# Kernel tuning notes

Measured on AMD Instinct MI355X. Metric: run time of the kernel, lower is better.

Reference implementation:

```python
import jax, jax.numpy as jnp
import numpy as np

N_NODES = 20000
N_EDGES = 40000
MAX_NB = 6
N_ATOM_FEAT = 98
N_BOND_FEAT = 13
HIDDEN = 256
DEPTH = 4
INPUT_SIZE = N_ATOM_FEAT + N_BOND_FEAT  # 111, hmess width


def setup_inputs() -> dict:
    key = jax.random.key(0)
    ks = jax.random.split(key, 10)
    fnode = jax.random.normal(ks[0], (N_NODES, N_ATOM_FEAT), jnp.float32)
    # fmess: col0/col1 are src/dst node indices stored as floats, cols 2: are bond features
    idx = jax.random.randint(ks[1], (N_EDGES, 2), 0, N_NODES).astype(jnp.float32)
    bond = jax.random.normal(ks[2], (N_EDGES, N_BOND_FEAT), jnp.float32)
    fmess = jnp.concatenate([idx, bond], axis=1)  # [E, 2 + n_bond_feat]
    agraph = jax.random.randint(ks[3], (N_NODES, MAX_NB), 0, N_EDGES)
    bgraph = jax.random.randint(ks[4], (N_EDGES, MAX_NB), 0, N_EDGES)
    s = 0.02
    W_z_w = jax.random.normal(ks[5], (HIDDEN, INPUT_SIZE + HIDDEN), jnp.float32) * s
    W_z_b = jnp.zeros((HIDDEN,), jnp.float32)
    W_r_w = jax.random.normal(ks[6], (HIDDEN, INPUT_SIZE), jnp.float32) * s  # no bias (W_r)
    U_r_w = jax.random.normal(ks[7], (HIDDEN, HIDDEN), jnp.float32) * s
    U_r_b = jnp.zeros((HIDDEN,), jnp.float32)
    W_h_w = jax.random.normal(ks[8], (HIDDEN, INPUT_SIZE + HIDDEN), jnp.float32) * s
    W_h_b = jnp.zeros((HIDDEN,), jnp.float32)
    W_o_w = jax.random.normal(ks[9], (HIDDEN, N_ATOM_FEAT + HIDDEN), jnp.float32) * s
    W_o_b = jnp.zeros((HIDDEN,), jnp.float32)
    return dict(fnode=fnode, fmess=fmess, agraph=agraph, bgraph=bgraph,
                W_z_w=W_z_w, W_z_b=W_z_b, W_r_w=W_r_w, U_r_w=U_r_w, U_r_b=U_r_b,
                W_h_w=W_h_w, W_h_b=W_h_b, W_o_w=W_o_w, W_o_b=W_o_b)


def reference(fnode, fmess, agraph, bgraph,
              W_z_w, W_z_b, W_r_w, U_r_w, U_r_b, W_h_w, W_h_b, W_o_w, W_o_b):
    # GraphFeatEncoder: gather src-node features and concat with bond features
    src = fmess[:, 0].astype(jnp.int32)
    x = jnp.concatenate([fnode[src], fmess[:, 2:]], axis=-1)  # [E, input_size]
    E = x.shape[0]
    H = W_z_b.shape[0]
    emask = jnp.ones((E, 1), x.dtype).at[0, 0].set(0.0)  # message 0 is padding
    Wr_x = (x @ W_r_w.T)[:, None, :]  # [E,1,H], constant across depth iterations
    h = jnp.zeros((E, H), x.dtype)
    # DGCNGRU: D-MPNN style GRU over directed-edge states
    for _ in range(DEPTH):
        h_nei = h[bgraph]                                   # [E, max_nb, H] gather
        sum_h = h_nei.sum(axis=1)                           # [E, H]
        z = jax.nn.sigmoid(jnp.concatenate([x, sum_h], axis=1) @ W_z_w.T + W_z_b)
        r = jax.nn.sigmoid(Wr_x + h_nei @ U_r_w.T + U_r_b)  # [E, max_nb, H]
        sum_gh = (r * h_nei).sum(axis=1)
        pre_h = jnp.tanh(jnp.concatenate([x, sum_gh], axis=1) @ W_h_w.T + W_h_b)
        h = ((1.0 - z) * sum_h + z * pre_h) * emask
    # DGCNEncoder readout: aggregate incoming edge states per atom
    nei_msg = h[agraph].sum(axis=1)                          # [N, H] gather + sum
    node_h = jax.nn.gelu(jnp.concatenate([fnode, nei_msg], axis=1) @ W_o_w.T + W_o_b,
                         approximate=False)                  # torch nn.GELU = exact erf
    nmask = jnp.ones((node_h.shape[0], 1), node_h.dtype).at[0, 0].set(0.0)  # node 0 pad
    hatom = node_h * nmask
    return hatom  # GraphFeatEncoder returns (hatom, None); hmol is always None
```

## Files before the change

### kernel.cpp

```cpp
#include <hip/hip_runtime.h>
#include <cstddef>
#include <cstdint>

typedef unsigned short u16;
typedef unsigned int   u32;
typedef __bf16  bf16x8 __attribute__((ext_vector_type(8)));
typedef float   f32x4  __attribute__((ext_vector_type(4)));

#define DEV __device__ __forceinline__

DEV float b2f(u16 u) { union { u32 i; float f; } c; c.i = ((u32)u) << 16; return c.f; }
DEV u16 f2b(float x) { union { float f; u32 i; } c; c.f = x; u32 b = c.i;
                       return (u16)((b + 0x7FFFu + ((b >> 16) & 1u)) >> 16); }
DEV float sigm(float x)  { return 1.0f / (1.0f + __expf(-x)); }
DEV float tanh_(float x) { return 1.0f - 2.0f / (1.0f + __expf(2.0f * x)); }
DEV float gelu_(float x) { return 0.5f * x * (1.0f + erff(x * 0.70710678118654752f)); }

DEV void u4tof8(uint4 v, float* f) {
    f[0] = b2f((u16)(v.x & 0xFFFF)); f[1] = b2f((u16)(v.x >> 16));
    f[2] = b2f((u16)(v.y & 0xFFFF)); f[3] = b2f((u16)(v.y >> 16));
    f[4] = b2f((u16)(v.z & 0xFFFF)); f[5] = b2f((u16)(v.z >> 16));
    f[6] = b2f((u16)(v.w & 0xFFFF)); f[7] = b2f((u16)(v.w >> 16));
}
DEV uint4 f8tou4(const float* f) {
    uint4 v;
    v.x = (u32)f2b(f[0]) | ((u32)f2b(f[1]) << 16);
    v.y = (u32)f2b(f[2]) | ((u32)f2b(f[3]) << 16);
    v.z = (u32)f2b(f[4]) | ((u32)f2b(f[5]) << 16);
    v.w = (u32)f2b(f[6]) | ((u32)f2b(f[7]) << 16);
    return v;
}

#define OB_X     0ull
#define OB_FB    10240000ull
#define OB_PRU   15360000ull
#define OB_H     35840000ull
#define OB_UH    56320000ull
#define OB_SH    76800000ull
#define OB_SGH   97280000ull
#define OB_BZ    117760000ull
#define OB_BH    117956608ull
#define OB_BU    118153216ull
#define OB_BR    118284288ull
#define OB_BO    118349824ull
#define WS_BYTES 118546432ull

__global__ __launch_bounds__(256) void k_repack(
    const float* __restrict__ Wz, const float* __restrict__ Wr,
    const float* __restrict__ Ur, const float* __restrict__ Wh,
    const float* __restrict__ Wo,
    u16* __restrict__ BzT, u16* __restrict__ BhT, u16* __restrict__ BuT,
    u16* __restrict__ BrT, u16* __restrict__ BoT) {
    int idx = blockIdx.x * 256 + threadIdx.x;
    {
        int n = idx / 384, k = idx % 384;
        float vz, vh, vo;
        if (k < 111)      { vz = Wz[n * 367 + k];          vh = Wh[n * 367 + k]; }
        else if (k < 128) { vz = 0.0f;                     vh = 0.0f; }
        else              { vz = Wz[n * 367 + k - 17];     vh = Wh[n * 367 + k - 17]; }
        if (k < 98)       vo = Wo[n * 354 + k];
        else if (k < 128) vo = 0.0f;
        else              vo = Wo[n * 354 + k - 30];
        BzT[idx] = f2b(vz); BhT[idx] = f2b(vh); BoT[idx] = f2b(vo);
    }
    if (idx < 65536) {
        BuT[idx] = f2b(Ur[idx]);
    }
    if (idx < 32768) {
        int n = idx >> 7, k = idx & 127;
        BrT[idx] = f2b(k < 111 ? Wr[n * 111 + k] : 0.0f);
    }
}

__global__ void k_build_x(const float* __restrict__ fnode,
                          const float* __restrict__ fmess, u16* __restrict__ x) {
    int e = blockIdx.x, c = threadIdx.x;
    int src = (int)fmess[(size_t)e * 15];
    float v = 0.0f;
    if (c < 98)       v = fnode[(size_t)src * 98 + c];
    else if (c < 111) v = fmess[(size_t)e * 15 + 2 + (c - 98)];
    x[(size_t)e * 128 + c] = f2b(v);
}

__global__ __launch_bounds__(256) void k_build_fb(const float* __restrict__ fnode,
                                                  u16* __restrict__ fb) {
    int idx = blockIdx.x * 256 + threadIdx.x;
    int n = idx >> 7, c = idx & 127;
    fb[idx] = f2b(c < 98 ? fnode[(size_t)n * 98 + c] : 0.0f);
}

DEV void stage128x64(const u16* __restrict__ g, size_t row0, int ld, int k0,
                     u16* s, int tid) {
    #pragma unroll
    for (int it = 0; it < 4; ++it) {
        int r = it * 32 + (tid >> 3);
        int c = (tid & 7) << 3;
        uint4 v = *(const uint4*)(g + (row0 + (size_t)r) * ld + k0 + c);
        int byte = (((r << 6) + c) << 1) ^ ((r & 7) << 4);
        *(uint4*)((char*)s + byte) = v;
    }
}

DEV void mma64s(const u16* As, const u16* Bs, f32x4 acc[4][4], int wr, int wc, int lane) {
    int rb = (wr << 6) + (lane & 15);
    int cb = (wc << 6) + (lane & 15);
    int ko = (lane >> 4) << 3;
    #pragma unroll
    for (int kh = 0; kh < 2; ++kh) {
        bf16x8 a[4], b[4];
        #pragma unroll
        for (int i = 0; i < 4; ++i) {
            int ar = rb + (i << 4);
            int ab = (((ar << 6) + (kh << 5) + ko) << 1) ^ ((ar & 7) << 4);
            a[i] = *(const bf16x8*)((const char*)As + ab);
            int br = cb + (i << 4);
            int bb = (((br << 6) + (kh << 5) + ko) << 1) ^ ((br & 7) << 4);
            b[i] = *(const bf16x8*)((const char*)Bs + bb);
        }
        #pragma unroll
        for (int i = 0; i < 4; ++i)
            #pragma unroll
            for (int j = 0; j < 4; ++j)
                acc[i][j] = __builtin_amdgcn_mfma_f32_16x16x32_bf16(b[j], a[i], acc[i][j], 0, 0, 0);
    }
}

#define MG_PROLOG()                                          \
    int tid = threadIdx.x, lane = tid & 63, w = tid >> 6;    \
    int wr = w >> 1, wc = w & 1;                             \
    int bm = blockIdx.x >> 1, bn = blockIdx.x & 1;           \
    size_t m0 = (size_t)bm << 7; int n0 = bn << 7;           \
    int row_l = (wr << 6) + (lane & 15);                     \
    int col_l = (wc << 6) + ((lane >> 4) << 2);

#define ACC_INIT(A)                                          \
    { f32x4 zz = {0.f, 0.f, 0.f, 0.f};                       \
      _Pragma("unroll") for (int i = 0; i < 4; ++i)          \
      _Pragma("unroll") for (int j = 0; j < 4; ++j) A[i][j] = zz; }

__global__ __launch_bounds__(256) void k_mg_p(
    const u16* __restrict__ x, const u16* __restrict__ BrT,
    const float* __restrict__ urb, u16* __restrict__ PrU) {
    __shared__ u16 As[8192], Bs[8192];
    MG_PROLOG()
    f32x4 acc[4][4]; ACC_INIT(acc)
    for (int k0 = 0; k0 < 128; k0 += 64) {
        __syncthreads();
        stage128x64(x, m0, 128, k0, As, tid);
        stage128x64(BrT, (size_t)n0, 128, k0, Bs, tid);
        __syncthreads();
        mma64s(As, Bs, acc, wr, wc, lane);
    }
    #pragma unroll
    for (int mi = 0; mi < 4; ++mi) {
        int m = (int)m0 + row_l + (mi << 4);
        if (m >= 40000) continue;
        #pragma unroll
        for (int ni = 0; ni < 4; ++ni) {
            int col = n0 + col_l + (ni << 4);
            float4 ub = *(const float4*)(urb + col);
            ushort4 o;
            o.x = f2b(acc[mi][ni][0] + ub.x); o.y = f2b(acc[mi][ni][1] + ub.y);
            o.z = f2b(acc[mi][ni][2] + ub.z); o.w = f2b(acc[mi][ni][3] + ub.w);
            *(ushort4*)(PrU + (size_t)m * 256 + col) = o;
        }
    }
}

__global__ __launch_bounds__(256) void k_d1(
    const u16* __restrict__ x, const u16* __restrict__ BzT,
    const u16* __restrict__ BhT, const float* __restrict__ bz,
    const float* __restrict__ bh, u16* __restrict__ h) {
    __shared__ u16 As[8192], Bs1[8192], Bs2[8192];
    MG_PROLOG()
    f32x4 aZ[4][4], aH[4][4]; ACC_INIT(aZ) ACC_INIT(aH)
    for (int k0 = 0; k0 < 128; k0 += 64) {
        __syncthreads();
        stage128x64(x, m0, 128, k0, As, tid);
        stage128x64(BzT, (size_t)n0, 384, k0, Bs1, tid);
        stage128x64(BhT, (size_t)n0, 384, k0, Bs2, tid);
        __syncthreads();
        mma64s(As, Bs1, aZ, wr, wc, lane);
        mma64s(As, Bs2, aH, wr, wc, lane);
    }
    #pragma unroll
    for (int mi = 0; mi < 4; ++mi) {
        int m = (int)m0 + row_l + (mi << 4);
        if (m >= 40000) continue;
        #pragma unroll
        for (int ni = 0; ni < 4; ++ni) {
            int col = n0 + col_l + (ni << 4);
            float4 vz = *(const float4*)(bz + col);
            float4 vh = *(const float4*)(bh + col);
            float r[4];
            r[0] = sigm(aZ[mi][ni][0] + vz.x) * tanh_(aH[mi][ni][0] + vh.x);
            r[1] = sigm(aZ[mi][ni][1] + vz.y) * tanh_(aH[mi][ni][1] + vh.y);
            r[2] = sigm(aZ[mi][ni][2] + vz.z) * tanh_(aH[mi][ni][2] + vh.z);
            r[3] = sigm(aZ[mi][ni][3] + vz.w) * tanh_(aH[mi][ni][3] + vh.w);
            if (m == 0) { r[0] = r[1] = r[2] = r[3] = 0.0f; }
            ushort4 o;
            o.x = f2b(r[0]); o.y = f2b(r[1]); o.z = f2b(r[2]); o.w = f2b(r[3]);
            *(ushort4*)(h + (size_t)m * 256 + col) = o;
        }
    }
}

__global__ __launch_bounds__(256) void k_mg_uh(
    const u16* __restrict__ A, const u16* __restrict__ BT, u16* __restrict__ C) {
    __shared__ u16 As[8192], Bs[8192];
    MG_PROLOG()
    f32x4 acc[4][4]; ACC_INIT(acc)
    for (int k0 = 0; k0 < 256; k0 += 64) {
        __syncthreads();
        stage128x64(A, m0, 256, k0, As, tid);
        stage128x64(BT, (size_t)n0, 256, k0, Bs, tid);
        __syncthreads();
        mma64s(As, Bs, acc, wr, wc, lane);
    }
    #pragma unroll
    for (int mi = 0; mi < 4; ++mi) {
        int m = (int)m0 + row_l + (mi << 4);
        if (m >= 40000) continue;
        #pragma unroll
        for (int ni = 0; ni < 4; ++ni) {
            int col = n0 + col_l + (ni << 4);
            ushort4 o;
            o.x = f2b(acc[mi][ni][0]); o.y = f2b(acc[mi][ni][1]);
            o.z = f2b(acc[mi][ni][2]); o.w = f2b(acc[mi][ni][3]);
            *(ushort4*)(C + (size_t)m * 256 + col) = o;
        }
    }
}

__global__ __launch_bounds__(256) void k_mg_fused(
    const u16* __restrict__ x, const u16* __restrict__ sumh,
    const u16* __restrict__ sumgh, const u16* __restrict__ BzT,
    const u16* __restrict__ BhT, const float* __restrict__ bz,
    const float* __restrict__ bh, u16* __restrict__ h) {
    __shared__ u16 As1[8192], As2[8192], Bs1[8192], Bs2[8192];
    MG_PROLOG()
    f32x4 aZ[4][4], aH[4][4]; ACC_INIT(aZ) ACC_INIT(aH)
    for (int s = 0; s < 6; ++s) {
        int k0 = s << 6;
        __syncthreads();
        if (s < 2) {
            stage128x64(x, m0, 128, k0, As1, tid);
        } else {
            stage128x64(sumh,  m0, 256, k0 - 128, As1, tid);
            stage128x64(sumgh, m0, 256, k0 - 128, As2, tid);
        }
        stage128x64(BzT, (size_t)n0, 384, k0, Bs1, tid);
        stage128x64(BhT, (size_t)n0, 384, k0, Bs2, tid);
        __syncthreads();
        mma64s(As1, Bs1, aZ, wr, wc, lane);
        mma64s(s < 2 ? As1 : As2, Bs2, aH, wr, wc, lane);
    }
    #pragma unroll
    for (int mi = 0; mi < 4; ++mi) {
        int m = (int)m0 + row_l + (mi << 4);
        if (m >= 40000) continue;
        #pragma unroll
        for (int ni = 0; ni < 4; ++ni) {
            int col = n0 + col_l + (ni << 4);
            float4 vz = *(const float4*)(bz + col);
            float4 vh = *(const float4*)(bh + col);
            ushort4 sh4 = *(const ushort4*)(sumh + (size_t)m * 256 + col);
            float shv[4] = {b2f(sh4.x), b2f(sh4.y), b2f(sh4.z), b2f(sh4.w)};
            float bzv[4] = {vz.x, vz.y, vz.z, vz.w};
            float bhv[4] = {vh.x, vh.y, vh.z, vh.w};
            float o[4];
            #pragma unroll
            for (int q = 0; q < 4; ++q) {
                float z   = sigm(aZ[mi][ni][q] + bzv[q]);
                float pre = tanh_(aH[mi][ni][q] + bhv[q]);
                o[q] = (1.0f - z) * shv[q] + z * pre;
            }
            if (m == 0) { o[0] = o[1] = o[2] = o[3] = 0.0f; }
            ushort4 ov;
            ov.x = f2b(o[0]); ov.y = f2b(o[1]); ov.z = f2b(o[2]); ov.w = f2b(o[3]);
            *(ushort4*)(h + (size_t)m * 256 + col) = ov;
        }
    }
}

__global__ __launch_bounds__(256) void k_mg_out(
    const u16* __restrict__ fb, const u16* __restrict__ nei,
    const u16* __restrict__ BoT, const float* __restrict__ bo,
    float* __restrict__ out) {
    __shared__ u16 As[8192], Bs[8192];
    MG_PROLOG()
    f32x4 acc[4][4]; ACC_INIT(acc)
    for (int s = 0; s < 6; ++s) {
        int k0 = s << 6;
        __syncthreads();
        if (s < 2) stage128x64(fb,  m0, 128, k0, As, tid);
        else       stage128x64(nei, m0, 256, k0 - 128, As, tid);
        stage128x64(BoT, (size_t)n0, 384, k0, Bs, tid);
        __syncthreads();
        mma64s(As, Bs, acc, wr, wc, lane);
    }
    #pragma unroll
    for (int mi = 0; mi < 4; ++mi) {
        int m = (int)m0 + row_l + (mi << 4);
        if (m >= 20000) continue;
        #pragma unroll
        for (int ni = 0; ni < 4; ++ni) {
            int col = n0 + col_l + (ni << 4);
            float4 vb = *(const float4*)(bo + col);
            float4 o;
            o.x = gelu_(acc[mi][ni][0] + vb.x);
            o.y = gelu_(acc[mi][ni][1] + vb.y);
            o.z = gelu_(acc[mi][ni][2] + vb.z);
            o.w = gelu_(acc[mi][ni][3] + vb.w);
            if (m == 0) { o.x = o.y = o.z = o.w = 0.0f; }
            *(float4*)(out + (size_t)m * 256 + col) = o;
        }
    }
}

__global__ __launch_bounds__(256) void k_gather_edge(
    const u16* __restrict__ h, const u16* __restrict__ Uh,
    const u16* __restrict__ PrU, const int* __restrict__ bgraph,
    u16* __restrict__ sumh, u16* __restrict__ sumgh) {
    int e = (blockIdx.x << 3) + (threadIdx.x >> 5);
    int c = (threadIdx.x & 31) << 3;
    size_t o = (size_t)e * 256 + c;
    float pr[8];
    u4tof8(*(const uint4*)(PrU + o), pr);
    float sh[8] = {}, sg[8] = {};
    #pragma unroll
    for (int j = 0; j < 6; ++j) {
        int b = bgraph[e * 6 + j];
        float hv[8], uv[8];
        u4tof8(*(const uint4*)(h  + (size_t)b * 256 + c), hv);
        u4tof8(*(const uint4*)(Uh + (size_t)b * 256 + c), uv);
        #pragma unroll
        for (int q = 0; q < 8; ++q) {
            sh[q] += hv[q];
            sg[q] += sigm(pr[q] + uv[q]) * hv[q];
        }
    }
    *(uint4*)(sumh  + o) = f8tou4(sh);
    *(uint4*)(sumgh + o) = f8tou4(sg);
}

__global__ __launch_bounds__(256) void k_gather_node(
    const u16* __restrict__ h, const int* __restrict__ agraph,
    u16* __restrict__ nei) {
    int n = (blockIdx.x << 3) + (threadIdx.x >> 5);
    int c = (threadIdx.x & 31) << 3;
    float s[8] = {};
    #pragma unroll
    for (int j = 0; j < 6; ++j) {
        int a = agraph[n * 6 + j];
        float hv[8];
        u4tof8(*(const uint4*)(h + (size_t)a * 256 + c), hv);
        #pragma unroll
        for (int q = 0; q < 8; ++q) s[q] += hv[q];
    }
    *(uint4*)(nei + (size_t)n * 256 + c) = f8tou4(s);
}

extern "C" void kernel_launch(void* const* d_in, const int* in_sizes, int n_in,
                              void* d_out, int out_size, void* d_ws, size_t ws_size,
                              hipStream_t stream) {
    if (ws_size < WS_BYTES) return;

    const float* fnode  = (const float*)d_in[0];
    const float* fmess  = (const float*)d_in[1];
    const int*   agraph = (const int*)d_in[2];
    const int*   bgraph = (const int*)d_in[3];
    const float* Wz  = (const float*)d_in[4];
    const float* bz  = (const float*)d_in[5];
    const float* Wr  = (const float*)d_in[6];
    const float* Ur  = (const float*)d_in[7];
    const float* urb = (const float*)d_in[8];
    const float* Wh  = (const float*)d_in[9];
    const float* bh  = (const float*)d_in[10];
    const float* Wo  = (const float*)d_in[11];
    const float* bo  = (const float*)d_in[12];

    char* base = (char*)d_ws;
    u16* x     = (u16*)(base + OB_X);
    u16* fb    = (u16*)(base + OB_FB);
    u16* PrU   = (u16*)(base + OB_PRU);
    u16* h     = (u16*)(base + OB_H);
    u16* Uh    = (u16*)(base + OB_UH);
    u16* nei   = (u16*)(base + OB_UH);
    u16* sumh  = (u16*)(base + OB_SH);
    u16* sumgh = (u16*)(base + OB_SGH);
    u16* BzT   = (u16*)(base + OB_BZ);
    u16* BhT   = (u16*)(base + OB_BH);
    u16* BuT   = (u16*)(base + OB_BU);
    u16* BrT   = (u16*)(base + OB_BR);
    u16* BoT   = (u16*)(base + OB_BO);
    float* out = (float*)d_out;

    hipLaunchKernelGGL(k_repack, dim3(384), dim3(256), 0, stream,
                       Wz, Wr, Ur, Wh, Wo, BzT, BhT, BuT, BrT, BoT);
    hipLaunchKernelGGL(k_build_x, dim3(40000), dim3(128), 0, stream, fnode, fmess, x);
    hipLaunchKernelGGL(k_build_fb, dim3(10000), dim3(256), 0, stream, fnode, fb);
    hipLaunchKernelGGL(k_mg_p, dim3(313 * 2), dim3(256), 0, stream, x, BrT, urb, PrU);
    hipLaunchKernelGGL(k_d1,   dim3(313 * 2), dim3(256), 0, stream, x, BzT, BhT, bz, bh, h);
    for (int d = 1; d < 4; ++d) {
        hipLaunchKernelGGL(k_mg_uh, dim3(313 * 2), dim3(256), 0, stream, h, BuT, Uh);
        hipLaunchKernelGGL(k_gather_edge, dim3(5000), dim3(256), 0, stream,
                           h, Uh, PrU, bgraph, sumh, sumgh);
        hipLaunchKernelGGL(k_mg_fused, dim3(313 * 2), dim3(256), 0, stream,
                           x, sumh, sumgh, BzT, BhT, bz, bh, h);
    }
    hipLaunchKernelGGL(k_gather_node, dim3(2500), dim3(256), 0, stream, h, agraph, nei);
    hipLaunchKernelGGL(k_mg_out, dim3(157 * 2), dim3(256), 0, stream, fb, nei, BoT, bo, out);
}
```

Baseline: 500.3 us.

## Use 128x64 GEMM tiles with register-prefetched global loads across all matmul kernels

```diff
diff --git a/kernel.cpp b/kernel.cpp
--- a/kernel.cpp
+++ b/kernel.cpp
@@ -55,26 +55,26 @@
     {
         int n = idx / 384, k = idx % 384;
         float vz, vh, vo;
-        if (k < 111)      { vz = Wz[n * 367 + k];          vh = Wh[n * 367 + k]; }
-        else if (k < 128) { vz = 0.0f;                     vh = 0.0f; }
-        else              { vz = Wz[n * 367 + k - 17];     vh = Wh[n * 367 + k - 17]; }
+        if (k < 111)      { vz = Wz[n * 367 + k];      vh = Wh[n * 367 + k]; }
+        else if (k < 128) { vz = 0.0f;                 vh = 0.0f; }
+        else              { vz = Wz[n * 367 + k - 17]; vh = Wh[n * 367 + k - 17]; }
         if (k < 98)       vo = Wo[n * 354 + k];
         else if (k < 128) vo = 0.0f;
         else              vo = Wo[n * 354 + k - 30];
         BzT[idx] = f2b(vz); BhT[idx] = f2b(vh); BoT[idx] = f2b(vo);
     }
-    if (idx < 65536) {
-        BuT[idx] = f2b(Ur[idx]);
-    }
+    if (idx < 65536) BuT[idx] = f2b(Ur[idx]);
     if (idx < 32768) {
         int n = idx >> 7, k = idx & 127;
         BrT[idx] = f2b(k < 111 ? Wr[n * 111 + k] : 0.0f);
     }
 }
 
-__global__ void k_build_x(const float* __restrict__ fnode,
-                          const float* __restrict__ fmess, u16* __restrict__ x) {
-    int e = blockIdx.x, c = threadIdx.x;
+__global__ __launch_bounds__(256) void k_build_x(const float* __restrict__ fnode,
+                                                 const float* __restrict__ fmess,
+                                                 u16* __restrict__ x) {
+    int e = (blockIdx.x << 1) + (threadIdx.x >> 7);
+    int c = threadIdx.x & 127;
     int src = (int)fmess[(size_t)e * 15];
     float v = 0.0f;
     if (c < 98)       v = fnode[(size_t)src * 98 + c];
@@ -89,178 +89,116 @@
     fb[idx] = f2b(c < 98 ? fnode[(size_t)n * 98 + c] : 0.0f);
 }
 
-DEV void stage128x64(const u16* __restrict__ g, size_t row0, int ld, int k0,
-                     u16* s, int tid) {
+DEV void ldA(const u16* __restrict__ g, size_t row0, int ld, int k0, int tid, uint4* v) {
     #pragma unroll
     for (int it = 0; it < 4; ++it) {
         int r = it * 32 + (tid >> 3);
         int c = (tid & 7) << 3;
-        uint4 v = *(const uint4*)(g + (row0 + (size_t)r) * ld + k0 + c);
+        v[it] = *(const uint4*)(g + (row0 + (size_t)r) * ld + k0 + c);
+    }
+}
+DEV void ldB(const u16* __restrict__ g, size_t row0, int ld, int k0, int tid, uint4* v) {
+    #pragma unroll
+    for (int it = 0; it < 2; ++it) {
+        int r = it * 32 + (tid >> 3);
+        int c = (tid & 7) << 3;
+        v[it] = *(const uint4*)(g + (row0 + (size_t)r) * ld + k0 + c);
+    }
+}
+DEV void wrA(u16* s, int tid, const uint4* v) {
+    #pragma unroll
+    for (int it = 0; it < 4; ++it) {
+        int r = it * 32 + (tid >> 3);
+        int c = (tid & 7) << 3;
         int byte = (((r << 6) + c) << 1) ^ ((r & 7) << 4);
-        *(uint4*)((char*)s + byte) = v;
-    }
-}
-
-DEV void mma64s(const u16* As, const u16* Bs, f32x4 acc[4][4], int wr, int wc, int lane) {
+        *(uint4*)((char*)s + byte) = v[it];
+    }
+}
+DEV void wrB(u16* s, int tid, const uint4* v) {
+    #pragma unroll
+    for (int it = 0; it < 2; ++it) {
+        int r = it * 32 + (tid >> 3);
+        int c = (tid & 7) << 3;
+        int byte = (((r << 6) + c) << 1) ^ ((r & 7) << 4);
+        *(uint4*)((char*)s + byte) = v[it];
+    }
+}
+DEV void mma_step(const u16* As, const u16* Bs, f32x4 acc[4][2], int lane, int wr, int wc) {
     int rb = (wr << 6) + (lane & 15);
-    int cb = (wc << 6) + (lane & 15);
+    int cb = (wc << 5) + (lane & 15);
     int ko = (lane >> 4) << 3;
     #pragma unroll
     for (int kh = 0; kh < 2; ++kh) {
-        bf16x8 a[4], b[4];
+        bf16x8 a[4], b[2];
         #pragma unroll
         for (int i = 0; i < 4; ++i) {
             int ar = rb + (i << 4);
-            int ab = (((ar << 6) + (kh << 5) + ko) << 1) ^ ((ar & 7) << 4);
-            a[i] = *(const bf16x8*)((const char*)As + ab);
-            int br = cb + (i << 4);
-            int bb = (((br << 6) + (kh << 5) + ko) << 1) ^ ((br & 7) << 4);
-            b[i] = *(const bf16x8*)((const char*)Bs + bb);
+            a[i] = *(const bf16x8*)((const char*)As +
+                   ((((ar << 6) + (kh << 5) + ko) << 1) ^ ((ar & 7) << 4)));
+        }
+        #pragma unroll
+        for (int j = 0; j < 2; ++j) {
+            int br = cb + (j << 4);
+            b[j] = *(const bf16x8*)((const char*)Bs +
+                   ((((br << 6) + (kh << 5) + ko) << 1) ^ ((br & 7) << 4)));
         }
         #pragma unroll
         for (int i = 0; i < 4; ++i)
             #pragma unroll
-            for (int j = 0; j < 4; ++j)
+            for (int j = 0; j < 2; ++j)
                 acc[i][j] = __builtin_amdgcn_mfma_f32_16x16x32_bf16(b[j], a[i], acc[i][j], 0, 0, 0);
     }
 }
 
-#define MG_PROLOG()                                          \
-    int tid = threadIdx.x, lane = tid & 63, w = tid >> 6;    \
-    int wr = w >> 1, wc = w & 1;                             \
-    int bm = blockIdx.x >> 1, bn = blockIdx.x & 1;           \
-    size_t m0 = (size_t)bm << 7; int n0 = bn << 7;           \
-    int row_l = (wr << 6) + (lane & 15);                     \
-    int col_l = (wc << 6) + ((lane >> 4) << 2);
-
-#define ACC_INIT(A)                                          \
-    { f32x4 zz = {0.f, 0.f, 0.f, 0.f};                       \
-      _Pragma("unroll") for (int i = 0; i < 4; ++i)          \
-      _Pragma("unroll") for (int j = 0; j < 4; ++j) A[i][j] = zz; }
-
-__global__ __launch_bounds__(256) void k_mg_p(
-    const u16* __restrict__ x, const u16* __restrict__ BrT,
-    const float* __restrict__ urb, u16* __restrict__ PrU) {
-    __shared__ u16 As[8192], Bs[8192];
-    MG_PROLOG()
-    f32x4 acc[4][4]; ACC_INIT(acc)
-    for (int k0 = 0; k0 < 128; k0 += 64) {
-        __syncthreads();
-        stage128x64(x, m0, 128, k0, As, tid);
-        stage128x64(BrT, (size_t)n0, 128, k0, Bs, tid);
-        __syncthreads();
-        mma64s(As, Bs, acc, wr, wc, lane);
-    }
-    #pragma unroll
-    for (int mi = 0; mi < 4; ++mi) {
-        int m = (int)m0 + row_l + (mi << 4);
-        if (m >= 40000) continue;
-        #pragma unroll
-        for (int ni = 0; ni < 4; ++ni) {
-            int col = n0 + col_l + (ni << 4);
-            float4 ub = *(const float4*)(urb + col);
-            ushort4 o;
-            o.x = f2b(acc[mi][ni][0] + ub.x); o.y = f2b(acc[mi][ni][1] + ub.y);
-            o.z = f2b(acc[mi][ni][2] + ub.z); o.w = f2b(acc[mi][ni][3] + ub.w);
-            *(ushort4*)(PrU + (size_t)m * 256 + col) = o;
-        }
-    }
-}
-
-__global__ __launch_bounds__(256) void k_d1(
-    const u16* __restrict__ x, const u16* __restrict__ BzT,
-    const u16* __restrict__ BhT, const float* __restrict__ bz,
-    const float* __restrict__ bh, u16* __restrict__ h) {
-    __shared__ u16 As[8192], Bs1[8192], Bs2[8192];
-    MG_PROLOG()
-    f32x4 aZ[4][4], aH[4][4]; ACC_INIT(aZ) ACC_INIT(aH)
-    for (int k0 = 0; k0 < 128; k0 += 64) {
-        __syncthreads();
-        stage128x64(x, m0, 128, k0, As, tid);
-        stage128x64(BzT, (size_t)n0, 384, k0, Bs1, tid);
-        stage128x64(BhT, (size_t)n0, 384, k0, Bs2, tid);
-        __syncthreads();
-        mma64s(As, Bs1, aZ, wr, wc, lane);
-        mma64s(As, Bs2, aH, wr, wc, lane);
-    }
-    #pragma unroll
-    for (int mi = 0; mi < 4; ++mi) {
-        int m = (int)m0 + row_l + (mi << 4);
-        if (m >= 40000) continue;
-        #pragma unroll
-        for (int ni = 0; ni < 4; ++ni) {
-            int col = n0 + col_l + (ni << 4);
-            float4 vz = *(const float4*)(bz + col);
-            float4 vh = *(const float4*)(bh + col);
-            float r[4];
-            r[0] = sigm(aZ[mi][ni][0] + vz.x) * tanh_(aH[mi][ni][0] + vh.x);
-            r[1] = sigm(aZ[mi][ni][1] + vz.y) * tanh_(aH[mi][ni][1] + vh.y);
-            r[2] = sigm(aZ[mi][ni][2] + vz.z) * tanh_(aH[mi][ni][2] + vh.z);
-            r[3] = sigm(aZ[mi][ni][3] + vz.w) * tanh_(aH[mi][ni][3] + vh.w);
-            if (m == 0) { r[0] = r[1] = r[2] = r[3] = 0.0f; }
-            ushort4 o;
-            o.x = f2b(r[0]); o.y = f2b(r[1]); o.z = f2b(r[2]); o.w = f2b(r[3]);
-            *(ushort4*)(h + (size_t)m * 256 + col) = o;
-        }
-    }
-}
-
-__global__ __launch_bounds__(256) void k_mg_uh(
-    const u16* __restrict__ A, const u16* __restrict__ BT, u16* __restrict__ C) {
-    __shared__ u16 As[8192], Bs[8192];
-    MG_PROLOG()
-    f32x4 acc[4][4]; ACC_INIT(acc)
-    for (int k0 = 0; k0 < 256; k0 += 64) {
-        __syncthreads();
-        stage128x64(A, m0, 256, k0, As, tid);
-        stage128x64(BT, (size_t)n0, 256, k0, Bs, tid);
-        __syncthreads();
-        mma64s(As, Bs, acc, wr, wc, lane);
-    }
-    #pragma unroll
-    for (int mi = 0; mi < 4; ++mi) {
-        int m = (int)m0 + row_l + (mi << 4);
-        if (m >= 40000) continue;
-        #pragma unroll
-        for (int ni = 0; ni < 4; ++ni) {
-            int col = n0 + col_l + (ni << 4);
-            ushort4 o;
-            o.x = f2b(acc[mi][ni][0]); o.y = f2b(acc[mi][ni][1]);
-            o.z = f2b(acc[mi][ni][2]); o.w = f2b(acc[mi][ni][3]);
-            *(ushort4*)(C + (size_t)m * 256 + col) = o;
-        }
-    }
-}
+#define GT_PROLOG()                                            \
+    __shared__ u16 As[8192], Bs[4096];                         \
+    int tid = threadIdx.x, lane = tid & 63, w = tid >> 6;      \
+    int wr = w >> 1, wc = w & 1;                               \
+    int bm = blockIdx.x >> 2, bn = blockIdx.x & 3;             \
+    size_t m0 = (size_t)bm << 7; int n0 = bn << 6;             \
+    int row_l = (wr << 6) + (lane & 15);                       \
+    int col_l = (wc << 5) + ((lane >> 4) << 2);                \
+    uint4 ra[4], rb_[2];
+
+#define ACC_INIT(A)                                            \
+    { f32x4 zz = {0.f, 0.f, 0.f, 0.f};                         \
+      _Pragma("unroll") for (int i = 0; i < 4; ++i)            \
+      _Pragma("unroll") for (int j = 0; j < 2; ++j) A[i][j] = zz; }
 
 __global__ __launch_bounds__(256) void k_mg_fused(
     const u16* __restrict__ x, const u16* __restrict__ sumh,
     const u16* __restrict__ sumgh, const u16* __restrict__ BzT,
     const u16* __restrict__ BhT, const float* __restrict__ bz,
     const float* __restrict__ bh, u16* __restrict__ h) {
-    __shared__ u16 As1[8192], As2[8192], Bs1[8192], Bs2[8192];
-    MG_PROLOG()
-    f32x4 aZ[4][4], aH[4][4]; ACC_INIT(aZ) ACC_INIT(aH)
-    for (int s = 0; s < 6; ++s) {
-        int k0 = s << 6;
+    GT_PROLOG()
+    f32x4 aZ[4][2], aH[4][2]; ACC_INIT(aZ) ACC_INIT(aH)
+    #define F_LD(t)                                                            \
+        { int tt = (t);                                                        \
+          if (tt < 2)      { ldA(x,     m0, 128, tt << 6, tid, ra);            \
+                             ldB(BzT, (size_t)n0, 384, tt << 6, tid, rb_); }   \
+          else if (tt < 4) { ldA(x,     m0, 128, (tt - 2) << 6, tid, ra);      \
+                             ldB(BhT, (size_t)n0, 384, (tt - 2) << 6, tid, rb_); } \
+          else if (tt < 8) { ldA(sumh,  m0, 256, (tt - 4) << 6, tid, ra);      \
+                             ldB(BzT, (size_t)n0, 384, 128 + ((tt - 4) << 6), tid, rb_); } \
+          else             { ldA(sumgh, m0, 256, (tt - 8) << 6, tid, ra);      \
+                             ldB(BhT, (size_t)n0, 384, 128 + ((tt - 8) << 6), tid, rb_); } }
+    F_LD(0)
+    for (int t = 0; t < 12; ++t) {
+        if (t) __syncthreads();
+        wrA(As, tid, ra); wrB(Bs, tid, rb_);
+        bool toH = (t >= 2 && t < 4) || (t >= 8);
         __syncthreads();
-        if (s < 2) {
-            stage128x64(x, m0, 128, k0, As1, tid);
-        } else {
-            stage128x64(sumh,  m0, 256, k0 - 128, As1, tid);
-            stage128x64(sumgh, m0, 256, k0 - 128, As2, tid);
-        }
-        stage128x64(BzT, (size_t)n0, 384, k0, Bs1, tid);
-        stage128x64(BhT, (size_t)n0, 384, k0, Bs2, tid);
-        __syncthreads();
-        mma64s(As1, Bs1, aZ, wr, wc, lane);
-        mma64s(s < 2 ? As1 : As2, Bs2, aH, wr, wc, lane);
-    }
+        if (t + 1 < 12) F_LD(t + 1)
+        if (toH) mma_step(As, Bs, aH, lane, wr, wc);
+        else     mma_step(As, Bs, aZ, lane, wr, wc);
+    }
+    #undef F_LD
     #pragma unroll
     for (int mi = 0; mi < 4; ++mi) {
         int m = (int)m0 + row_l + (mi << 4);
         if (m >= 40000) continue;
         #pragma unroll
-        for (int ni = 0; ni < 4; ++ni) {
+        for (int ni = 0; ni < 2; ++ni) {
             int col = n0 + col_l + (ni << 4);
             float4 vz = *(const float4*)(bz + col);
             float4 vh = *(const float4*)(bh + col);
@@ -283,28 +221,133 @@
     }
 }
 
+__global__ __launch_bounds__(256) void k_mg_uh(
+    const u16* __restrict__ A, const u16* __restrict__ BT, u16* __restrict__ C) {
+    GT_PROLOG()
+    f32x4 acc[4][2]; ACC_INIT(acc)
+    ldA(A, m0, 256, 0, tid, ra); ldB(BT, (size_t)n0, 256, 0, tid, rb_);
+    for (int t = 0; t < 4; ++t) {
+        if (t) __syncthreads();
+        wrA(As, tid, ra); wrB(Bs, tid, rb_);
+        __syncthreads();
+        if (t + 1 < 4) { ldA(A, m0, 256, (t + 1) << 6, tid, ra);
+                         ldB(BT, (size_t)n0, 256, (t + 1) << 6, tid, rb_); }
+        mma_step(As, Bs, acc, lane, wr, wc);
+    }
+    #pragma unroll
+    for (int mi = 0; mi < 4; ++mi) {
+        int m = (int)m0 + row_l + (mi << 4);
+        if (m >= 40000) continue;
+        #pragma unroll
+        for (int ni = 0; ni < 2; ++ni) {
+            int col = n0 + col_l + (ni << 4);
+            ushort4 o;
+            o.x = f2b(acc[mi][ni][0]); o.y = f2b(acc[mi][ni][1]);
+            o.z = f2b(acc[mi][ni][2]); o.w = f2b(acc[mi][ni][3]);
+            *(ushort4*)(C + (size_t)m * 256 + col) = o;
+        }
+    }
+}
+
+__global__ __launch_bounds__(256) void k_mg_p(
+    const u16* __restrict__ x, const u16* __restrict__ BrT,
+    const float* __restrict__ urb, u16* __restrict__ PrU) {
+    GT_PROLOG()
+    f32x4 acc[4][2]; ACC_INIT(acc)
+    ldA(x, m0, 128, 0, tid, ra); ldB(BrT, (size_t)n0, 128, 0, tid, rb_);
+    for (int t = 0; t < 2; ++t) {
+        if (t) __syncthreads();
+        wrA(As, tid, ra); wrB(Bs, tid, rb_);
+        __syncthreads();
+        if (t + 1 < 2) { ldA(x, m0, 128, 64, tid, ra);
+                         ldB(BrT, (size_t)n0, 128, 64, tid, rb_); }
+        mma_step(As, Bs, acc, lane, wr, wc);
+    }
+    #pragma unroll
+    for (int mi = 0; mi < 4; ++mi) {
+        int m = (int)m0 + row_l + (mi << 4);
+        if (m >= 40000) continue;
+        #pragma unroll
+        for (int ni = 0; ni < 2; ++ni) {
+            int col = n0 + col_l + (ni << 4);
+            float4 ub = *(const float4*)(urb + col);
+            ushort4 o;
+            o.x = f2b(acc[mi][ni][0] + ub.x); o.y = f2b(acc[mi][ni][1] + ub.y);
+            o.z = f2b(acc[mi][ni][2] + ub.z); o.w = f2b(acc[mi][ni][3] + ub.w);
+            *(ushort4*)(PrU + (size_t)m * 256 + col) = o;
+        }
+    }
+}
+
+__global__ __launch_bounds__(256) void k_d1(
+    const u16* __restrict__ x, const u16* __restrict__ BzT,
+    const u16* __restrict__ BhT, const float* __restrict__ bz,
+    const float* __restrict__ bh, u16* __restrict__ h) {
+    GT_PROLOG()
+    f32x4 aZ[4][2], aH[4][2]; ACC_INIT(aZ) ACC_INIT(aH)
+    #define D_LD(t)                                                           \
+        { int tt = (t);                                                       \
+          ldA(x, m0, 128, (tt & 1) << 6, tid, ra);                            \
+          ldB(tt < 2 ? BzT : BhT, (size_t)n0, 384, (tt & 1) << 6, tid, rb_); }
+    D_LD(0)
+    for (int t = 0; t < 4; ++t) {
+        if (t) __syncthreads();
+        wrA(As, tid, ra); wrB(Bs, tid, rb_);
+        __syncthreads();
+        if (t + 1 < 4) D_LD(t + 1)
+        if (t < 2) mma_step(As, Bs, aZ, lane, wr, wc);
+        else       mma_step(As, Bs, aH, lane, wr, wc);
+    }
+    #undef D_LD
+    #pragma unroll
+    for (int mi = 0; mi < 4; ++mi) {
+        int m = (int)m0 + row_l + (mi << 4);
+        if (m >= 40000) continue;
+        #pragma unroll
+        for (int ni = 0; ni < 2; ++ni) {
+            int col = n0 + col_l + (ni << 4);
+            float4 vz = *(const float4*)(bz + col);
+            float4 vh = *(const float4*)(bh + col);
+            float r[4];
+            r[0] = sigm(aZ[mi][ni][0] + vz.x) * tanh_(aH[mi][ni][0] + vh.x);
+            r[1] = sigm(aZ[mi][ni][1] + vz.y) * tanh_(aH[mi][ni][1] + vh.y);
+            r[2] = sigm(aZ[mi][ni][2] + vz.z) * tanh_(aH[mi][ni][2] + vh.z);
+            r[3] = sigm(aZ[mi][ni][3] + vz.w) * tanh_(aH[mi][ni][3] + vh.w);
+            if (m == 0) { r[0] = r[1] = r[2] = r[3] = 0.0f; }
+            ushort4 o;
+            o.x = f2b(r[0]); o.y = f2b(r[1]); o.z = f2b(r[2]); o.w = f2b(r[3]);
+            *(ushort4*)(h + (size_t)m * 256 + col) = o;
+        }
+    }
+}
+
 __global__ __launch_bounds__(256) void k_mg_out(
     const u16* __restrict__ fb, const u16* __restrict__ nei,
     const u16* __restrict__ BoT, const float* __restrict__ bo,
     float* __restrict__ out) {
-    __shared__ u16 As[8192], Bs[8192];
-    MG_PROLOG()
-    f32x4 acc[4][4]; ACC_INIT(acc)
-    for (int s = 0; s < 6; ++s) {
-        int k0 = s << 6;
+    GT_PROLOG()
+    f32x4 acc[4][2]; ACC_INIT(acc)
+    #define O_LD(t)                                                           \
+        { int tt = (t);                                                       \
+          if (tt < 2) { ldA(fb,  m0, 128, tt << 6, tid, ra);                  \
+                        ldB(BoT, (size_t)n0, 384, tt << 6, tid, rb_); }       \
+          else        { ldA(nei, m0, 256, (tt - 2) << 6, tid, ra);            \
+                        ldB(BoT, (size_t)n0, 384, 128 + ((tt - 2) << 6), tid, rb_); } }
+    O_LD(0)
+    for (int t = 0; t < 6; ++t) {
+        if (t) __syncthreads();
+        wrA(As, tid, ra); wrB(Bs, tid, rb_);
         __syncthreads();
-        if (s < 2) stage128x64(fb,  m0, 128, k0, As, tid);
-        else       stage128x64(nei, m0, 256, k0 - 128, As, tid);
-        stage128x64(BoT, (size_t)n0, 384, k0, Bs, tid);
-        __syncthreads();
-        mma64s(As, Bs, acc, wr, wc, lane);
-    }
+        if (t + 1 < 6) O_LD(t + 1)
+        mma_step(As, Bs, acc, lane, wr, wc);
+    }
+    #undef O_LD
     #pragma unroll
     for (int mi = 0; mi < 4; ++mi) {
         int m = (int)m0 + row_l + (mi << 4);
         if (m >= 20000) continue;
         #pragma unroll
-        for (int ni = 0; ni < 4; ++ni) {
+        for (int ni = 0; ni < 2; ++ni) {
             int col = n0 + col_l + (ni << 4);
             float4 vb = *(const float4*)(bo + col);
             float4 o;
@@ -398,17 +441,17 @@
 
     hipLaunchKernelGGL(k_repack, dim3(384), dim3(256), 0, stream,
                        Wz, Wr, Ur, Wh, Wo, BzT, BhT, BuT, BrT, BoT);
-    hipLaunchKernelGGL(k_build_x, dim3(40000), dim3(128), 0, stream, fnode, fmess, x);
+    hipLaunchKernelGGL(k_build_x, dim3(20000), dim3(256), 0, stream, fnode, fmess, x);
     hipLaunchKernelGGL(k_build_fb, dim3(10000), dim3(256), 0, stream, fnode, fb);
-    hipLaunchKernelGGL(k_mg_p, dim3(313 * 2), dim3(256), 0, stream, x, BrT, urb, PrU);
-    hipLaunchKernelGGL(k_d1,   dim3(313 * 2), dim3(256), 0, stream, x, BzT, BhT, bz, bh, h);
+    hipLaunchKernelGGL(k_mg_p, dim3(1252), dim3(256), 0, stream, x, BrT, urb, PrU);
+    hipLaunchKernelGGL(k_d1,   dim3(1252), dim3(256), 0, stream, x, BzT, BhT, bz, bh, h);
     for (int d = 1; d < 4; ++d) {
-        hipLaunchKernelGGL(k_mg_uh, dim3(313 * 2), dim3(256), 0, stream, h, BuT, Uh);
+        hipLaunchKernelGGL(k_mg_uh, dim3(1252), dim3(256), 0, stream, h, BuT, Uh);
         hipLaunchKernelGGL(k_gather_edge, dim3(5000), dim3(256), 0, stream,
                            h, Uh, PrU, bgraph, sumh, sumgh);
-        hipLaunchKernelGGL(k_mg_fused, dim3(313 * 2), dim3(256), 0, stream,
+        hipLaunchKernelGGL(k_mg_fused, dim3(1252), dim3(256), 0, stream,
                            x, sumh, sumgh, BzT, BhT, bz, bh, h);
     }
     hipLaunchKernelGGL(k_gather_node, dim3(2500), dim3(256), 0, stream, h, agraph, nei);
-    hipLaunchKernelGGL(k_mg_out, dim3(157 * 2), dim3(256), 0, stream, fb, nei, BoT, bo, out);
-}
+    hipLaunchKernelGGL(k_mg_out, dim3(628), dim3(256), 0, stream, fb, nei, BoT, bo, out);
+}
```

Measured after the change: 773.3 us. 1.55x slower.
